# Performance work log

Measured on AMD Instinct MI355X. Metric: run time of the kernel, lower is better.

## Reference

```python
import jax, jax.numpy as jnp
import numpy as np

B, T, E = 64, 512, 768
H = 512            # hid_dim
NF = 256           # n_filters
FS = (3, 4, 5)     # filter_sizes


def gru_step(x, h, Wih, Whh, bih, bhh):
    # torch.nn.GRUCell math; gate order: reset, update, new
    gi = x @ Wih.T + bih
    gh = h @ Whh.T + bhh
    ir, iz, in_ = jnp.split(gi, 3, axis=-1)
    hr, hz, hn = jnp.split(gh, 3, axis=-1)
    r = jax.nn.sigmoid(ir + hr)
    z = jax.nn.sigmoid(iz + hz)
    n = jnp.tanh(in_ + r * hn)
    return (1.0 - z) * n + z * h


def setup_inputs() -> dict:
    key = jax.random.key(0)
    ks = jax.random.split(key, 32)
    s = 0.02
    inp = {
        "embedded": jax.random.normal(ks[0], (B, T, E), jnp.float32),
        "mask": jnp.ones((B, T), jnp.int32),
        # select-policy GRUCell
        "Wih_c": jax.random.normal(ks[1], (3 * H, E)) * s,
        "Whh_c": jax.random.normal(ks[2], (3 * H, H)) * s,
        "bih_c": jnp.zeros((3 * H,)),
        "bhh_c": jnp.zeros((3 * H,)),
        "Ws": jax.random.normal(ks[3], (2, H)) * s,
        "bs": jnp.zeros((2,)),
        # 2-layer GRU
        "Wih0": jax.random.normal(ks[4], (3 * H, E)) * s,
        "Whh0": jax.random.normal(ks[5], (3 * H, H)) * s,
        "bih0": jnp.zeros((3 * H,)),
        "bhh0": jnp.zeros((3 * H,)),
        "Wih1": jax.random.normal(ks[6], (3 * H, H)) * s,
        "Whh1": jax.random.normal(ks[7], (3 * H, H)) * s,
        "bih1": jnp.zeros((3 * H,)),
        "bhh1": jnp.zeros((3 * H,)),
        # convs (OIHW)
        "Wc3": jax.random.normal(ks[8], (NF, 1, 3, H)) * s,
        "bc3": jnp.zeros((NF,)),
        "Wc4": jax.random.normal(ks[9], (NF, 1, 4, H)) * s,
        "bc4": jnp.zeros((NF,)),
        "Wc5": jax.random.normal(ks[10], (NF, 1, 5, H)) * s,
        "bc5": jnp.zeros((NF,)),
        # output linear
        "Wo": jax.random.normal(ks[11], (1, len(FS) * NF)) * s,
        "bo": jnp.zeros((1,)),
    }
    return inp


def reference(embedded, mask, Wih_c, Whh_c, bih_c, bhh_c, Ws, bs,
              Wih0, Whh0, bih0, bhh0, Wih1, Whh1, bih1, bhh1,
              Wc3, bc3, Wc4, bc4, Wc5, bc5, Wo, bo):
    b, t, _ = embedded.shape
    emb = jax.lax.stop_gradient(embedded)  # policy uses detached embeddings
    lens = mask.sum(axis=1).astype(jnp.int32)  # [B]

    # --- select_policy (eval mode: argmax selection), batched scan over time ---
    def sel_step(h, x_t):
        h = gru_step(x_t, h, Wih_c, Whh_c, bih_c, bhh_c)
        logits = h @ Ws.T + bs  # [B, 2]
        return h, jnp.argmax(logits, axis=-1).astype(jnp.int32)

    h0 = jnp.zeros((b, Whh_c.shape[1]), emb.dtype)
    _, ks = jax.lax.scan(sel_step, h0, jnp.swapaxes(emb, 0, 1))  # [T, B]
    sel = ks.T  # [B, T]
    t_idx = jnp.arange(t)[None, :]
    sel = jnp.where(t_idx == 0, 1, sel)                  # first token always kept
    sel = jnp.where(t_idx == lens[:, None] - 1, 1, sel)  # last valid token kept
    sel = jnp.where(t_idx >= lens[:, None], 0, sel)      # padding never kept
    nsel = sel.sum(axis=1)  # [B] lengths of compacted sequences

    # compact selected tokens to the front (stable argsort trick)
    order = jnp.argsort(1 - sel, axis=1, stable=True)  # [B, T]
    new_emb = jnp.take_along_axis(emb, order[:, :, None], axis=1)
    valid = t_idx < nsel[:, None]  # [B, T]
    new_emb = new_emb * valid[:, :, None].astype(emb.dtype)

    # --- 2-layer GRU over packed (= masked, left-aligned) sequences ---
    def run_layer(x, Wih, Whh, bih, bhh):
        def step(h, inputs):
            x_t, m_t = inputs
            hn = gru_step(x_t, h, Wih, Whh, bih, bhh)
            h = jnp.where(m_t[:, None], hn, h)
            return h, jnp.where(m_t[:, None], hn, jnp.zeros_like(hn))
        hh = jnp.zeros((x.shape[0], Whh.shape[1]), x.dtype)
        _, ys = jax.lax.scan(step, hh, (jnp.swapaxes(x, 0, 1), valid.T))
        return jnp.swapaxes(ys, 0, 1)  # [B, T, H]

    out = run_layer(new_emb, Wih0, Whh0, bih0, bhh0)
    out = run_layer(out, Wih1, Whh1, bih1, bhh1)

    # --- Kim-CNN head ---
    xc = out[:, None, :, :]  # [B, 1, T, H]
    pooled = []
    for Wc, bc in ((Wc3, bc3), (Wc4, bc4), (Wc5, bc5)):
        c = jax.lax.conv_general_dilated(
            xc, Wc, (1, 1), 'VALID',
            dimension_numbers=('NCHW', 'OIHW', 'NCHW'))  # [B, NF, T-fs+1, 1]
        c = jax.nn.relu(c + bc[None, :, None, None])[..., 0]
        pooled.append(jnp.max(c, axis=2))  # [B, NF]
    cat = jnp.concatenate(pooled, axis=1)  # dropout is identity in eval
    return (cat @ Wo.T + bo)[:, 0]  # [B]
```

## Files before the change

### kernel.cpp

```cpp
#include <hip/hip_runtime.h>
#include <hip/hip_bf16.h>
#include <cstddef>

constexpr int B_ = 64, T_ = 512, E_ = 768, H_ = 512, G_ = 1536, NF_ = 256;

typedef float f32x4 __attribute__((ext_vector_type(4)));
typedef __bf16 bf16x8 __attribute__((ext_vector_type(8)));

constexpr size_t SZ_GIC   = (size_t)B_ * T_ * G_ * 4;
constexpr size_t OFF_GI   = 0;
constexpr size_t OFF_OUT  = (size_t)B_ * T_ * G_ * 2;
constexpr size_t OFF_WBF0 = 170u * 1024 * 1024;
constexpr size_t OFF_WBF1 = OFF_WBF0 + (size_t)G_ * H_ * 2;
constexpr size_t OFF_WIH0 = OFF_WBF1 + (size_t)G_ * H_ * 2;
constexpr size_t OFF_WIH1 = OFF_WIH0 + (size_t)G_ * E_ * 2;
constexpr size_t OFF_WC3  = OFF_WIH1 + (size_t)G_ * H_ * 2;
constexpr size_t OFF_WC4  = OFF_WC3 + (size_t)NF_ * 3 * H_ * 2;
constexpr size_t OFF_WC5  = OFF_WC4 + (size_t)NF_ * 4 * H_ * 2;
constexpr size_t OFF_MISC = SZ_GIC;
constexpr size_t OFF_H0   = OFF_MISC;
constexpr size_t OFF_H1   = OFF_H0 + (size_t)B_ * H_ * 4;
constexpr size_t OFF_SEL  = OFF_H1 + (size_t)B_ * H_ * 4;
constexpr size_t OFF_ORD  = OFF_SEL + (size_t)B_ * T_ * 4;
constexpr size_t OFF_NSEL = OFF_ORD + (size_t)B_ * T_ * 4;
constexpr size_t OFF_MAXN = OFF_NSEL + 256;
constexpr size_t OFF_FLG  = OFF_MAXN + 256;
constexpr size_t OFF_POOL = OFF_FLG + 512;
constexpr size_t OFF_RING0 = OFF_POOL + (size_t)B_ * 3 * NF_ * 4;
constexpr size_t OFF_RING1 = OFF_RING0 + 4ull * 64 * 512 * 2;
constexpr size_t WS_NEED  = OFF_RING1 + 4ull * 64 * 1536 * 2;

constexpr int WP_N0 = G_ * H_;
constexpr int WP_N1 = WP_N0 + G_ * H_;
constexpr int WP_N2 = WP_N1 + G_ * E_;
constexpr int WP_N3 = WP_N2 + G_ * H_;
constexpr int WP_N4 = WP_N3 + NF_ * 3 * H_;
constexpr int WP_N5 = WP_N4 + NF_ * 4 * H_;
constexpr int WP_N6 = WP_N5 + NF_ * 5 * H_;

#define CLOAD4(dst, ptr) \
    asm volatile("global_load_dwordx4 %0, %1, off sc0 sc1" : "=v"(dst) : "v"(ptr))
#define CLOAD2(dst, ptr) \
    asm volatile("global_load_dwordx2 %0, %1, off sc0 sc1" : "=v"(dst) : "v"(ptr))
#define CWAIT() do { \
    asm volatile("s_waitcnt vmcnt(0)" ::: "memory"); \
    __builtin_amdgcn_sched_barrier(0); } while (0)
#define CSTORE4(ptr, val) \
    asm volatile("global_store_dword %0, %1, off sc0 sc1" :: "v"(ptr), "v"(val) : "memory")
#define CSTORE8(ptr, val) \
    asm volatile("global_store_dwordx2 %0, %1, off sc0 sc1" :: "v"(ptr), "v"(val) : "memory")
#define CSTORE2(ptr, val) \
    asm volatile("global_store_short %0, %1, off sc0 sc1" :: "v"(ptr), "v"(val) : "memory")

__device__ __forceinline__ float sigm(float x) { return 1.f / (1.f + expf(-x)); }
__device__ __forceinline__ float b2f(unsigned short u) {
    return __uint_as_float(((unsigned int)u) << 16);
}
__device__ __forceinline__ unsigned short f2bu(float x) {
    __hip_bfloat16 h = __float2bfloat16(x);
    return *(unsigned short*)&h;
}

template<int NWG>
__device__ __forceinline__ void bar_wait(const int* flags, int t, int tid) {
    if (tid < 64) {
        int v;
        for (;;) {
            asm volatile("global_load_dword %0, %1, off sc0 sc1\n\t"
                         "s_waitcnt vmcnt(0)"
                         : "=v"(v) : "v"(flags + (tid & (NWG - 1))) : "memory");
            if (__all(v >= t)) break;
            __builtin_amdgcn_s_sleep(1);
        }
    }
    __syncthreads();
}

template<int N>
__device__ __forceinline__ void poll_ge(const int* flags, int thresh, int tid) {
    if (tid < 64) {
        const int idx = (tid < N) ? tid : 0;
        int v;
        for (;;) {
            asm volatile("global_load_dword %0, %1, off sc0 sc1\n\t"
                         "s_waitcnt vmcnt(0)"
                         : "=v"(v) : "v"(flags + idx) : "memory");
            if (__all(v >= thresh)) break;
            __builtin_amdgcn_s_sleep(1);
        }
    }
    __syncthreads();
}

__device__ __forceinline__ void bar_wait128(const int* flags, int t, int tid) {
    if (tid < 64) {
        int v1, v2;
        for (;;) {
            asm volatile("global_load_dword %0, %2, off sc0 sc1\n\t"
                         "global_load_dword %1, %3, off sc0 sc1\n\t"
                         "s_waitcnt vmcnt(0)"
                         : "=&v"(v1), "=&v"(v2)
                         : "v"(flags + tid), "v"(flags + tid + 64) : "memory");
            if (__all((v1 >= t) && (v2 >= t))) break;
            __builtin_amdgcn_s_sleep(1);
        }
    }
    __syncthreads();
}

__device__ __forceinline__ void bar_arrive(int* flags, int t, int tid, int idx) {
    asm volatile("s_waitcnt vmcnt(0)" ::: "memory");
    __syncthreads();
    if (tid == 0) { int pv = t + 1; CSTORE4(flags + idx, pv); }
}

__global__ __launch_bounds__(256) void gemm_f32(
    const float* __restrict__ A, const float* __restrict__ W,
    const float* __restrict__ bias, float* __restrict__ Cf,
    int N, int K, int ldA)
{
    __shared__ float As[16 * 68];
    __shared__ float Bs[16 * 68];
    const int tid = threadIdx.x;
    const int tx = tid & 15, ty = tid >> 4;
    const int id = blockIdx.x;
    const int sup = id / 384, rr = id % 384;
    const int bx = sup * 16 + (rr & 15);
    const int n0 = (rr >> 4) * 64;

    float acc[4][4] = {};
    const int rl = tid >> 2, kl = (tid & 3) * 4;
    const float* __restrict__ ap = A + ((size_t)bx * 64 + rl) * (size_t)ldA + kl;
    const float* __restrict__ wrow = W + (size_t)(n0 + rl) * (size_t)K + kl;

    for (int k0 = 0; k0 < K; k0 += 16) {
        float4 av = *(const float4*)(ap + k0);
        float4 wv = *(const float4*)(wrow + k0);
        __syncthreads();
        As[(kl+0)*68+rl] = av.x; As[(kl+1)*68+rl] = av.y;
        As[(kl+2)*68+rl] = av.z; As[(kl+3)*68+rl] = av.w;
        Bs[(kl+0)*68+rl] = wv.x; Bs[(kl+1)*68+rl] = wv.y;
        Bs[(kl+2)*68+rl] = wv.z; Bs[(kl+3)*68+rl] = wv.w;
        __syncthreads();
        #pragma unroll
        for (int kk = 0; kk < 16; ++kk) {
            const float4 a4 = *(const float4*)&As[kk*68 + ty*4];
            const float4 w4 = *(const float4*)&Bs[kk*68 + tx*4];
            acc[0][0]=fmaf(a4.x,w4.x,acc[0][0]); acc[0][1]=fmaf(a4.x,w4.y,acc[0][1]);
            acc[0][2]=fmaf(a4.x,w4.z,acc[0][2]); acc[0][3]=fmaf(a4.x,w4.w,acc[0][3]);
            acc[1][0]=fmaf(a4.y,w4.x,acc[1][0]); acc[1][1]=fmaf(a4.y,w4.y,acc[1][1]);
            acc[1][2]=fmaf(a4.y,w4.z,acc[1][2]); acc[1][3]=fmaf(a4.y,w4.w,acc[1][3]);
            acc[2][0]=fmaf(a4.z,w4.x,acc[2][0]); acc[2][1]=fmaf(a4.z,w4.y,acc[2][1]);
            acc[2][2]=fmaf(a4.z,w4.z,acc[2][2]); acc[2][3]=fmaf(a4.z,w4.w,acc[2][3]);
            acc[3][0]=fmaf(a4.w,w4.x,acc[3][0]); acc[3][1]=fmaf(a4.w,w4.y,acc[3][1]);
            acc[3][2]=fmaf(a4.w,w4.z,acc[3][2]); acc[3][3]=fmaf(a4.w,w4.w,acc[3][3]);
        }
    }
    #pragma unroll
    for (int i = 0; i < 4; ++i) {
        int m = bx * 64 + ty*4 + i;
        size_t co = (size_t)m * (size_t)N + n0 + tx*4;
        #pragma unroll
        for (int j = 0; j < 4; ++j)
            Cf[co + j] = acc[i][j] + bias[n0 + tx*4 + j];
    }
}

template<int AMODE, int OMODE>
__global__ __launch_bounds__(256) void gemm_mfma(
    const float* __restrict__ A, const unsigned short* __restrict__ Wb,
    const float* __restrict__ bias,
    unsigned short* __restrict__ Cb, unsigned int* __restrict__ pool,
    int N, int K, int ldA, int rowsPerB, int tilesPerB, int nb,
    const int* __restrict__ order, const int* __restrict__ nsel, int poolOff)
{
    __shared__ __align__(16) unsigned short As[64][40];
    __shared__ __align__(16) unsigned short Bs[64][40];
    __shared__ const float* rowp[64];

    const int tid = threadIdx.x;
    const int l = tid & 63;
    const int q = tid >> 6;
    const int per = 16 * nb;
    const int id = blockIdx.x;
    const int sup = id / per, rr2 = id % per;
    const int mblk = sup * 16 + (rr2 & 15);
    const int n0 = (rr2 >> 4) * 64;

    int tileb = 0, tilet0 = 0;
    if (AMODE != 0) { tileb = mblk / tilesPerB; tilet0 = (mblk % tilesPerB) * 64; }

    if (tid < 64) {
        const float* p = nullptr;
        if (AMODE == 0) {
            p = A + ((size_t)mblk * 64 + tid) * (size_t)ldA;
        } else if (AMODE == 1) {
            int t = tilet0 + tid;
            if (t < nsel[tileb]) {
                int src = order[tileb * T_ + t];
                p = A + ((size_t)tileb * T_ + src) * (size_t)ldA;
            }
        } else {
            int t = tilet0 + tid;
            if (t < rowsPerB) p = A + ((size_t)tileb * T_ + t) * (size_t)ldA;
        }
        rowp[tid] = p;
    }
    __syncthreads();

    f32x4 acc0 = {0.f,0.f,0.f,0.f}, acc1 = {0.f,0.f,0.f,0.f};
    f32x4 acc2 = {0.f,0.f,0.f,0.f}, acc3 = {0.f,0.f,0.f,0.f};

    const int r = tid & 63, seg = tid >> 6;
    const float* ap = rowp[r];
    if (ap) ap += seg * 8;
    const unsigned short* wrow = Wb + (size_t)(n0 + r) * (size_t)K + seg * 8;

    for (int k0 = 0; k0 < K; k0 += 32) {
        float4 fa = make_float4(0,0,0,0), fb = make_float4(0,0,0,0);
        if (ap) { fa = *(const float4*)(ap + k0); fb = *(const float4*)(ap + k0 + 4); }
        const uint4 wv = *(const uint4*)(wrow + k0);
        __syncthreads();
        uint4 pk;
        pk.x = (unsigned)f2bu(fa.x) | ((unsigned)f2bu(fa.y) << 16);
        pk.y = (unsigned)f2bu(fa.z) | ((unsigned)f2bu(fa.w) << 16);
        pk.z = (unsigned)f2bu(fb.x) | ((unsigned)f2bu(fb.y) << 16);
        pk.w = (unsigned)f2bu(fb.z) | ((unsigned)f2bu(fb.w) << 16);
        *(uint4*)&As[r][seg * 8] = pk;
        *(uint4*)&Bs[r][seg * 8] = wv;
        __syncthreads();
        const bf16x8 av = *(const bf16x8*)&As[q * 16 + (l & 15)][(l >> 4) * 8];
        const bf16x8 b0 = *(const bf16x8*)&Bs[ 0 + (l & 15)][(l >> 4) * 8];
        const bf16x8 b1 = *(const bf16x8*)&Bs[16 + (l & 15)][(l >> 4) * 8];
        const bf16x8 b2 = *(const bf16x8*)&Bs[32 + (l & 15)][(l >> 4) * 8];
        const bf16x8 b3 = *(const bf16x8*)&Bs[48 + (l & 15)][(l >> 4) * 8];
        acc0 = __builtin_amdgcn_mfma_f32_16x16x32_bf16(av, b0, acc0, 0, 0, 0);
        acc1 = __builtin_amdgcn_mfma_f32_16x16x32_bf16(av, b1, acc1, 0, 0, 0);
        acc2 = __builtin_amdgcn_mfma_f32_16x16x32_bf16(av, b2, acc2, 0, 0, 0);
        acc3 = __builtin_amdgcn_mfma_f32_16x16x32_bf16(av, b3, acc3, 0, 0, 0);
    }

    f32x4 accs[4] = {acc0, acc1, acc2, acc3};
    if (OMODE == 0) {
        const int mbase = (AMODE == 0) ? mblk * 64 : tileb * T_ + tilet0;
        #pragma unroll
        for (int s = 0; s < 4; ++s) {
            const int col = n0 + s * 16 + (l & 15);
            const float bv = bias[col];
            #pragma unroll
            for (int reg = 0; reg < 4; ++reg) {
                const int m = mbase + q * 16 + (l >> 4) * 4 + reg;
                Cb[(size_t)m * (size_t)N + col] = f2bu(accs[s][reg] + bv);
            }
        }
    } else {
        #pragma unroll
        for (int s = 0; s < 4; ++s) {
            const int col = n0 + s * 16 + (l & 15);
            const float bv = bias[col];
            float mx = 0.f;
            #pragma unroll
            for (int reg = 0; reg < 4; ++reg) {
                const int t = tilet0 + q * 16 + (l >> 4) * 4 + reg;
                const float val = fmaxf(accs[s][reg] + bv, 0.f);
                if (t < rowsPerB) mx = fmaxf(mx, val);
            }
            mx = fmaxf(mx, __shfl_xor(mx, 16));
            mx = fmaxf(mx, __shfl_xor(mx, 32));
            if (l < 16)
                atomicMax(&pool[(size_t)tileb * (3*NF_) + poolOff + n0 + s*16 + l],
                          __float_as_uint(mx));
        }
    }
}

__global__ void wprep_all(
    const float* __restrict__ w0, const float* __restrict__ w1,
    const float* __restrict__ w2, const float* __restrict__ w3,
    const float* __restrict__ w4, const float* __restrict__ w5,
    const float* __restrict__ w6, unsigned short* __restrict__ o)
{
    const int i = blockIdx.x * 256 + threadIdx.x;
    if (i >= WP_N6) return;
    float v;
    if      (i < WP_N0) v = w0[i];
    else if (i < WP_N1) v = w1[i - WP_N0];
    else if (i < WP_N2) v = w2[i - WP_N1];
    else if (i < WP_N3) v = w3[i - WP_N2];
    else if (i < WP_N4) v = w4[i - WP_N3];
    else if (i < WP_N5) v = w5[i - WP_N4];
    else                v = w6[i - WP_N5];
    o[i] = f2bu(v);
}

__device__ __forceinline__ void gates_abs(
    const float* __restrict__ hs, int b, int base,
    const float* __restrict__ wR, const float* __restrict__ wZ,
    const float* __restrict__ wN,
    float& aR, float& aZ, float& aN)
{
    #pragma unroll 4
    for (int kq = 0; kq < 32; ++kq) {
        const int k = base + kq * 4;
        const float hv0 = hs[(k+0)*64 + b];
        const float hv1 = hs[(k+1)*64 + b];
        const float hv2 = hs[(k+2)*64 + b];
        const float hv3 = hs[(k+3)*64 + b];
        const float4 wr = *(const float4*)(wR + k);
        const float4 wz = *(const float4*)(wZ + k);
        const float4 wn = *(const float4*)(wN + k);
        aR = fmaf(hv0, wr.x, aR); aR = fmaf(hv1, wr.y, aR);
        aR = fmaf(hv2, wr.z, aR); aR = fmaf(hv3, wr.w, aR);
        aZ = fmaf(hv0, wz.x, aZ); aZ = fmaf(hv1, wz.y, aZ);
        aZ = fmaf(hv2, wz.z, aZ); aZ = fmaf(hv3, wz.w, aZ);
        aN = fmaf(hv0, wn.x, aN); aN = fmaf(hv1, wn.y, aN);
        aN = fmaf(hv2, wn.z, aN); aN = fmaf(hv3, wn.w, aN);
    }
}

__device__ __forceinline__ void dot_abs(
    const float* __restrict__ hs, int b, int base,
    const float* __restrict__ dWl, float& dot)
{
    #pragma unroll 4
    for (int kq = 0; kq < 16; ++kq) {
        const int k = base + kq * 4;
        const float hv0 = hs[(k+0)*64 + b];
        const float hv1 = hs[(k+1)*64 + b];
        const float hv2 = hs[(k+2)*64 + b];
        const float hv3 = hs[(k+3)*64 + b];
        const float4 dv = *(const float4*)(dWl + k);
        dot = fmaf(hv0, dv.x, dot); dot = fmaf(hv1, dv.y, dot);
        dot = fmaf(hv2, dv.z, dot); dot = fmaf(hv3, dv.w, dot);
    }
}

__global__ __launch_bounds__(512) void rec_sel(
    const float* __restrict__ giF,
    const float* __restrict__ Whh, const float* __restrict__ bhh,
    const float* __restrict__ Ws, const float* __restrict__ bs,
    float* __restrict__ h0, float* __restrict__ h1,
    unsigned long long* __restrict__ selm, int* __restrict__ flags)
{
    __shared__ float Wl[12 * 512];
    __shared__ float dWl[512];
    __shared__ float hs[512 * 64];
    __shared__ float partR[4 * 64], partZ[4 * 64], partN[4 * 64];
    __shared__ float pdot[8 * 64];

    const int tid = threadIdx.x;
    const int b = tid & 63;
    const int w = __builtin_amdgcn_readfirstlane(tid >> 6);
    const int u = w >> 1, s = w & 1;
    const int bx = blockIdx.x;
    const int iu = bx * 4 + u;

    for (int idx = tid; idx < 12 * 512; idx += 512) {
        int rr = idx >> 9, k = idx & 511;
        int ul = rr / 3, gate = rr - ul * 3;
        Wl[idx] = Whh[((size_t)gate * 512 + bx * 4 + ul) * 512 + k];
    }
    dWl[tid] = Ws[512 + tid] - Ws[tid];
    __syncthreads();

    const float bR = bhh[iu], bZ = bhh[512 + iu], bN = bhh[1024 + iu];
    const float db = bs[1] - bs[0];
    const float* __restrict__ wR = Wl + (u*3 + 0) * 512;
    const float* __restrict__ wZ = Wl + (u*3 + 1) * 512;
    const float* __restrict__ wN = Wl + (u*3 + 2) * 512;

    float pgR = 0.f, pgZ = 0.f, pgN = 0.f;
    if (s == 0) {
        pgR = giF[(size_t)b * T_ * G_ + iu];
        pgZ = giF[(size_t)b * T_ * G_ + 512 + iu];
        pgN = giF[(size_t)b * T_ * G_ + 1024 + iu];
    }

    for (int t = 0; t <= T_; ++t) {
        const bool comp = (t < T_);
        const float* hcur = (t & 1) ? h1 : h0;
        float* hnxt = (t & 1) ? h0 : h1;

        if (t > 0) bar_wait128(flags, t, tid);

        const float* hc = hcur + (size_t)tid * 4;
        float* hd = hs + tid * 4;
        float4 a0,a1,a2,a3,a4,a5,a6,a7,a8,a9,aa,ab,ac,ad,ae,af;
        CLOAD4(a0, hc +  0*2048); CLOAD4(a1, hc +  1*2048);
        CLOAD4(a2, hc +  2*2048); CLOAD4(a3, hc +  3*2048);
        CLOAD4(a4, hc +  4*2048); CLOAD4(a5, hc +  5*2048);
        CLOAD4(a6, hc +  6*2048); CLOAD4(a7, hc +  7*2048);
        CLOAD4(a8, hc +  8*2048); CLOAD4(a9, hc +  9*2048);
        CLOAD4(aa, hc + 10*2048); CLOAD4(ab, hc + 11*2048);
        CLOAD4(ac, hc + 12*2048); CLOAD4(ad, hc + 13*2048);
        CLOAD4(ae, hc + 14*2048); CLOAD4(af, hc + 15*2048);
        CWAIT();
        *(float4*)(hd +  0*2048) = a0; *(float4*)(hd +  1*2048) = a1;
        *(float4*)(hd +  2*2048) = a2; *(float4*)(hd +  3*2048) = a3;
        *(float4*)(hd +  4*2048) = a4; *(float4*)(hd +  5*2048) = a5;
        *(float4*)(hd +  6*2048) = a6; *(float4*)(hd +  7*2048) = a7;
        *(float4*)(hd +  8*2048) = a8; *(float4*)(hd +  9*2048) = a9;
        *(float4*)(hd + 10*2048) = aa; *(float4*)(hd + 11*2048) = ab;
        *(float4*)(hd + 12*2048) = ac; *(float4*)(hd + 13*2048) = ad;
        *(float4*)(hd + 14*2048) = ae; *(float4*)(hd + 15*2048) = af;
        __syncthreads();

        float aR = (s == 0) ? bR : 0.f;
        float aZ = (s == 0) ? bZ : 0.f;
        float aN = (s == 0) ? bN : 0.f;
        float dot = 0.f, hp = 0.f;

        if (comp) {
            gates_abs(hs, b, s * 128,       wR, wZ, wN, aR, aZ, aN);
            gates_abs(hs, b, 256 + s * 128, wR, wZ, wN, aR, aZ, aN);
            if (s == 0) hp = hs[iu * 64 + b];
        }
        dot_abs(hs, b, (w < 4) ? w * 64 : 256 + (w - 4) * 64, dWl, dot);

        if (comp && s == 1) {
            partR[u*64 + b] = aR; partZ[u*64 + b] = aZ; partN[u*64 + b] = aN;
        }
        pdot[w*64 + b] = dot;
        __syncthreads();

        if (comp && s == 0) {
            aR += partR[u*64 + b]; aZ += partZ[u*64 + b]; aN += partN[u*64 + b];
            const float r = sigm(pgR + aR);
            const float z = sigm(pgZ + aZ);
            const float n = tanhf(pgN + r * aN);
            const float hn = (1.f - z) * n + z * hp;
            const float* hdst = hnxt + (size_t)iu * 64 + b;
            CSTORE4(hdst, hn);
        }

        if (t < T_) {
            bar_arrive(flags, t, tid, bx);
            if (s == 0 && t + 1 < T_) {
                const float* gp = giF + ((size_t)b * T_ + t + 1) * G_;
                pgR = gp[iu]; pgZ = gp[512 + iu]; pgN = gp[1024 + iu];
            }
        }
        if (w == 0 && t >= 1) {
            float p = pdot[0*64 + b];
            p += pdot[1*64 + b]; p += pdot[2*64 + b]; p += pdot[3*64 + b];
            p += pdot[4*64 + b]; p += pdot[5*64 + b]; p += pdot[6*64 + b];
            p += pdot[7*64 + b];
            unsigned long long m = __ballot((p + db) > 0.f);
            if (tid == 0 && bx == 0) selm[t - 1] = m;
        }
    }
}

template<int ROLE>
__device__ __forceinline__ void layer_body(
    int wg, int tid,
    const unsigned short* __restrict__ gi0,
    const unsigned short* __restrict__ ring1,
    unsigned short* __restrict__ ring0,
    const unsigned short* __restrict__ wbf, const float* __restrict__ bhh,
    const int* __restrict__ nselp, const int* __restrict__ maxnp,
    unsigned short* __restrict__ hA, unsigned short* __restrict__ hB,
    float* __restrict__ outp,
    int* __restrict__ flagsSelf, const int* __restrict__ flagsB,
    unsigned char* ldsW, unsigned char* ldsH, float* gbuf)
{
    const int l = tid & 63;
    const int q = tid >> 6;
    const int i0 = wg * 16;
    const int b = tid & 63;

    for (int idx = tid; idx < 48 * 64; idx += 256) {
        const int r = idx >> 6, seg = idx & 63;
        const int tier = r >> 4, ul = r & 15;
        const float4 v = *(const float4*)((const char*)wbf
            + ((size_t)(tier * 512 + i0 + ul) * 512) * 2 + seg * 16);
        *(float4*)(ldsW + r * 1040 + seg * 16) = v;
    }
    const float4 bRv = *(const float4*)(bhh + i0 + 4 * q);
    const float4 bZv = *(const float4*)(bhh + 512 + i0 + 4 * q);
    const float4 bNv = *(const float4*)(bhh + 1024 + i0 + 4 * q);
    const int ns = nselp[b];
    const int TOTAL = *maxnp;

    const unsigned short* gbase = gi0 + (size_t)b * T_ * (size_t)G_ + i0 + 4 * q;
    uint2 gR, gZ, gN;
    if (ROLE == 0) {
        gR = *(const uint2*)(gbase);
        gZ = *(const uint2*)(gbase + 512);
        gN = *(const uint2*)(gbase + 1024);
    }
    __syncthreads();

    for (int t = 0; t < TOTAL; ++t) {
        const unsigned short* hcur = (t & 1) ? hB : hA;
        unsigned short* hnxt = (t & 1) ? hA : hB;

        if (t > 0) bar_wait<32>(flagsSelf, t, tid);
        if (ROLE == 0) {
            if (t >= 4) poll_ge<24>(flagsB, t - 3, tid);
        } else {
            poll_ge<24>(flagsB, t + 1, tid);
            const unsigned short* gp = ring1 + ((size_t)(t & 3) * 64 + b) * G_ + i0 + 4 * q;
            CLOAD2(gR, gp); CLOAD2(gZ, gp + 512); CLOAD2(gN, gp + 1024);
        }

        {
            const char* src = (const char*)hcur + tid * 256;
            float4 s0, s1, s2, s3, s4, s5, s6, s7, s8, s9, sa, sb_, sc, sd, se, sf;
            CLOAD4(s0, src + 0 * 16);  CLOAD4(s1, src + 1 * 16);
            CLOAD4(s2, src + 2 * 16);  CLOAD4(s3, src + 3 * 16);
            CLOAD4(s4, src + 4 * 16);  CLOAD4(s5, src + 5 * 16);
            CLOAD4(s6, src + 6 * 16);  CLOAD4(s7, src + 7 * 16);
            CLOAD4(s8, src + 8 * 16);  CLOAD4(s9, src + 9 * 16);
            CLOAD4(sa, src + 10 * 16); CLOAD4(sb_, src + 11 * 16);
            CLOAD4(sc, src + 12 * 16); CLOAD4(sd, src + 13 * 16);
            CLOAD4(se, src + 14 * 16); CLOAD4(sf, src + 15 * 16);
            CWAIT();
            char* dst = (char*)ldsH + (tid >> 2) * 1040 + (tid & 3) * 256;
            *(float4*)(dst + 0 * 16) = s0;  *(float4*)(dst + 1 * 16) = s1;
            *(float4*)(dst + 2 * 16) = s2;  *(float4*)(dst + 3 * 16) = s3;
            *(float4*)(dst + 4 * 16) = s4;  *(float4*)(dst + 5 * 16) = s5;
            *(float4*)(dst + 6 * 16) = s6;  *(float4*)(dst + 7 * 16) = s7;
            *(float4*)(dst + 8 * 16) = s8;  *(float4*)(dst + 9 * 16) = s9;
            *(float4*)(dst + 10 * 16) = sa; *(float4*)(dst + 11 * 16) = sb_;
            *(float4*)(dst + 12 * 16) = sc; *(float4*)(dst + 13 * 16) = sd;
            *(float4*)(dst + 14 * 16) = se; *(float4*)(dst + 15 * 16) = sf;
        }
        __syncthreads();

        f32x4 ac0 = {0.f, 0.f, 0.f, 0.f};
        f32x4 ac1 = {0.f, 0.f, 0.f, 0.f};
        f32x4 ac2 = {0.f, 0.f, 0.f, 0.f};
        {
            const char* ab2 = (const char*)ldsH + (q * 16 + (l & 15)) * 1040 + (l >> 4) * 16;
            const char* bb = (const char*)ldsW + (l & 15) * 1040 + (l >> 4) * 16;
            #pragma unroll
            for (int ks = 0; ks < 16; ++ks) {
                const bf16x8 av = *(const bf16x8*)(ab2 + ks * 64);
                const bf16x8 w0 = *(const bf16x8*)(bb + ks * 64);
                const bf16x8 w1 = *(const bf16x8*)(bb + 16 * 1040 + ks * 64);
                const bf16x8 w2 = *(const bf16x8*)(bb + 32 * 1040 + ks * 64);
                ac0 = __builtin_amdgcn_mfma_f32_16x16x32_bf16(av, w0, ac0, 0, 0, 0);
                ac1 = __builtin_amdgcn_mfma_f32_16x16x32_bf16(av, w1, ac1, 0, 0, 0);
                ac2 = __builtin_amdgcn_mfma_f32_16x16x32_bf16(av, w2, ac2, 0, 0, 0);
            }
        }
        {
            const int gcol = q * 16 + 4 * (l >> 4);
            const int grow = l & 15;
            #pragma unroll
            for (int r = 0; r < 4; ++r) {
                gbuf[grow * 66 + gcol + r]        = ac0[r];
                gbuf[(16 + grow) * 66 + gcol + r] = ac1[r];
                gbuf[(32 + grow) * 66 + gcol + r] = ac2[r];
            }
        }
        __syncthreads();

        {
            const ushort4 hp4 = *(const ushort4*)((const char*)ldsH
                                 + b * 1040 + (i0 + 4 * q) * 2);
            const unsigned short hpb[4] = {hp4.x, hp4.y, hp4.z, hp4.w};
            const float irv[4] = {b2f(gR.x & 0xffff), b2f(gR.x >> 16),
                                  b2f(gR.y & 0xffff), b2f(gR.y >> 16)};
            const float izv[4] = {b2f(gZ.x & 0xffff), b2f(gZ.x >> 16),
                                  b2f(gZ.y & 0xffff), b2f(gZ.y >> 16)};
            const float inv[4] = {b2f(gN.x & 0xffff), b2f(gN.x >> 16),
                                  b2f(gN.y & 0xffff), b2f(gN.y >> 16)};
            float4 o;
            unsigned short ob[4];
            #pragma unroll
            for (int j = 0; j < 4; ++j) {
                const int u2 = 4 * q + j;
                const float hr = gbuf[u2 * 66 + b]        + bRv[j];
                const float hz = gbuf[(16 + u2) * 66 + b] + bZv[j];
                const float hn = gbuf[(32 + u2) * 66 + b] + bNv[j];
                const float rr = sigm(irv[j] + hr);
                const float zz = sigm(izv[j] + hz);
                const float nn = tanhf(inv[j] + rr * hn);
                const float hpf = b2f(hpb[j]);
                float hv = (1.f - zz) * nn + zz * hpf;
                if (t >= ns) hv = hpf;
                ((float*)&o)[j] = hv;
                ob[j] = f2bu(hv);
            }
            uint2 hpk;
            hpk.x = (unsigned)ob[0] | ((unsigned)ob[1] << 16);
            hpk.y = (unsigned)ob[2] | ((unsigned)ob[3] << 16);
            if (ROLE == 0) {
                const unsigned short* rdst = ring0 + ((size_t)(t & 3) * 64 + b) * 512 + i0 + 4 * q;
                CSTORE8(rdst, hpk);
            } else {
                if (t < ns)
                    *(float4*)(outp + ((size_t)b * T_ + t) * 512 + i0 + 4 * q) = o;
            }
            const unsigned short* hdst = hnxt + (size_t)b * 512 + i0 + 4 * q;
            CSTORE8(hdst, hpk);
        }

        bar_arrive(flagsSelf, t, tid, wg);
        if (ROLE == 0 && t + 1 < TOTAL) {
            const unsigned short* gp = gbase + (size_t)(t + 1) * G_;
            gR = *(const uint2*)gp;
            gZ = *(const uint2*)(gp + 512);
            gN = *(const uint2*)(gp + 1024);
        }
    }
}

__global__ __launch_bounds__(256) void rec_fused(
    const unsigned short* __restrict__ gi0,
    const unsigned short* __restrict__ wbf0,
    const unsigned short* __restrict__ wbf1,
    const unsigned short* __restrict__ wih1b,
    const float* __restrict__ bhh0, const float* __restrict__ bhh1,
    const float* __restrict__ bih1,
    const int* __restrict__ nselp, const int* __restrict__ maxnp,
    unsigned short* __restrict__ h0A, unsigned short* __restrict__ h1A,
    unsigned short* __restrict__ h0C, unsigned short* __restrict__ h1C,
    unsigned short* __restrict__ ring0, unsigned short* __restrict__ ring1,
    float* __restrict__ outp,
    int* __restrict__ flagsA, int* __restrict__ flagsB, int* __restrict__ flagsC)
{
    __shared__ __align__(16) unsigned char ldsX[64 * 1040];
    __shared__ __align__(16) unsigned char ldsY[64 * 1040];
    __shared__ float gbuf[48 * 66];

    const int tid = threadIdx.x;
    const int bx = blockIdx.x;

    if (bx < 32) {
        layer_body<0>(bx, tid, gi0, nullptr, ring0, wbf0, bhh0, nselp, maxnp,
                      h0A, h1A, nullptr, flagsA, flagsB, ldsX, ldsY, gbuf);
    } else if (bx < 56) {
        const int wg = bx - 32;
        const int l = tid & 63;
        const int q = tid >> 6;
        const int n0 = wg * 64;

        for (int idx = tid; idx < 64 * 64; idx += 256) {
            const int r = idx >> 6, seg = idx & 63;
            const float4 v = *(const float4*)((const char*)wih1b
                + ((size_t)(n0 + r) * 512) * 2 + seg * 16);
            *(float4*)(ldsX + r * 1040 + seg * 16) = v;
        }
        float bv[4];
        #pragma unroll
        for (int s = 0; s < 4; ++s) bv[s] = bih1[n0 + s * 16 + (l & 15)];
        const int TOTAL = *maxnp;
        __syncthreads();

        for (int t = 0; t < TOTAL; ++t) {
            poll_ge<32>(flagsA, t + 1, tid);
            if (t >= 4) poll_ge<32>(flagsC, t - 3, tid);

            {
                const char* src = (const char*)ring0 + (size_t)(t & 3) * 65536 + tid * 256;
                float4 s0, s1, s2, s3, s4, s5, s6, s7, s8, s9, sa, sb_, sc, sd, se, sf;
                CLOAD4(s0, src + 0 * 16);  CLOAD4(s1, src + 1 * 16);
                CLOAD4(s2, src + 2 * 16);  CLOAD4(s3, src + 3 * 16);
                CLOAD4(s4, src + 4 * 16);  CLOAD4(s5, src + 5 * 16);
                CLOAD4(s6, src + 6 * 16);  CLOAD4(s7, src + 7 * 16);
                CLOAD4(s8, src + 8 * 16);  CLOAD4(s9, src + 9 * 16);
                CLOAD4(sa, src + 10 * 16); CLOAD4(sb_, src + 11 * 16);
                CLOAD4(sc, src + 12 * 16); CLOAD4(sd, src + 13 * 16);
                CLOAD4(se, src + 14 * 16); CLOAD4(sf, src + 15 * 16);
                CWAIT();
                char* dst = (char*)ldsY + (tid >> 2) * 1040 + (tid & 3) * 256;
                *(float4*)(dst + 0 * 16) = s0;  *(float4*)(dst + 1 * 16) = s1;
                *(float4*)(dst + 2 * 16) = s2;  *(float4*)(dst + 3 * 16) = s3;
                *(float4*)(dst + 4 * 16) = s4;  *(float4*)(dst + 5 * 16) = s5;
                *(float4*)(dst + 6 * 16) = s6;  *(float4*)(dst + 7 * 16) = s7;
                *(float4*)(dst + 8 * 16) = s8;  *(float4*)(dst + 9 * 16) = s9;
                *(float4*)(dst + 10 * 16) = sa; *(float4*)(dst + 11 * 16) = sb_;
                *(float4*)(dst + 12 * 16) = sc; *(float4*)(dst + 13 * 16) = sd;
                *(float4*)(dst + 14 * 16) = se; *(float4*)(dst + 15 * 16) = sf;
            }
            __syncthreads();

            f32x4 acc0 = {0.f,0.f,0.f,0.f}, acc1 = {0.f,0.f,0.f,0.f};
            f32x4 acc2 = {0.f,0.f,0.f,0.f}, acc3 = {0.f,0.f,0.f,0.f};
            {
                const char* ab2 = (const char*)ldsY + (q * 16 + (l & 15)) * 1040 + (l >> 4) * 16;
                const char* bb = (const char*)ldsX + (l & 15) * 1040 + (l >> 4) * 16;
                #pragma unroll
                for (int ks = 0; ks < 16; ++ks) {
                    const bf16x8 av = *(const bf16x8*)(ab2 + ks * 64);
                    const bf16x8 b0 = *(const bf16x8*)(bb + ks * 64);
                    const bf16x8 b1 = *(const bf16x8*)(bb + 16 * 1040 + ks * 64);
                    const bf16x8 b2 = *(const bf16x8*)(bb + 32 * 1040 + ks * 64);
                    const bf16x8 b3 = *(const bf16x8*)(bb + 48 * 1040 + ks * 64);
                    acc0 = __builtin_amdgcn_mfma_f32_16x16x32_bf16(av, b0, acc0, 0, 0, 0);
                    acc1 = __builtin_amdgcn_mfma_f32_16x16x32_bf16(av, b1, acc1, 0, 0, 0);
                    acc2 = __builtin_amdgcn_mfma_f32_16x16x32_bf16(av, b2, acc2, 0, 0, 0);
                    acc3 = __builtin_amdgcn_mfma_f32_16x16x32_bf16(av, b3, acc3, 0, 0, 0);
                }
            }
            f32x4 accs[4] = {acc0, acc1, acc2, acc3};
            #pragma unroll
            for (int s = 0; s < 4; ++s) {
                const int col = n0 + s * 16 + (l & 15);
                #pragma unroll
                for (int reg = 0; reg < 4; ++reg) {
                    const int m = q * 16 + (l >> 4) * 4 + reg;
                    const unsigned val = f2bu(accs[s][reg] + bv[s]);
                    const unsigned short* dst = ring1 + ((size_t)(t & 3) * 64 + m) * G_ + col;
                    CSTORE2(dst, val);
                }
            }
            bar_arrive(flagsB, t, tid, wg);
        }
    } else {
        layer_body<1>(bx - 56, tid, nullptr, ring1, nullptr, wbf1, bhh1, nselp, maxnp,
                      h0C, h1C, outp, flagsC, flagsB, ldsX, ldsY, gbuf);
    }
}

__global__ void build_order_k(const int* __restrict__ mask,
                              const unsigned long long* __restrict__ selm,
                              int* __restrict__ order, int* __restrict__ nsel,
                              int* __restrict__ maxn)
{
    const int b = threadIdx.x;
    int lens = 0;
    for (int t = 0; t < T_; ++t) lens += (mask[b * T_ + t] != 0);
    int cnt = 0;
    for (int t = 0; t < T_; ++t) {
        int s = (int)((selm[t] >> b) & 1ull);
        if (t == 0) s = 1;
        if (t == lens - 1) s = 1;
        if (t >= lens) s = 0;
        if (s) order[b * T_ + (cnt++)] = t;
    }
    nsel[b] = cnt;
    int c2 = cnt;
    for (int t = 0; t < T_; ++t) {
        int s = (int)((selm[t] >> b) & 1ull);
        if (t == 0) s = 1;
        if (t == lens - 1) s = 1;
        if (t >= lens) s = 0;
        if (!s) order[b * T_ + (c2++)] = t;
    }
    __shared__ int red[64];
    red[b] = cnt;
    __syncthreads();
    if (b == 0) {
        int m = 0;
        for (int qq = 0; qq < 64; ++qq) m = max(m, red[qq]);
        *maxn = m;
    }
}

__global__ void final_k(const unsigned int* __restrict__ pool,
                        const float* __restrict__ Wo, const float* __restrict__ bo,
                        float* __restrict__ out)
{
    const int b = threadIdx.x;
    float s = bo[0];
    for (int f = 0; f < 3 * NF_; ++f)
        s = fmaf(__uint_as_float(pool[b * (3*NF_) + f]), Wo[f], s);
    out[b] = s;
}

extern "C" void kernel_launch(void* const* d_in, const int* in_sizes, int n_in,
                              void* d_out, int out_size, void* d_ws, size_t ws_size,
                              hipStream_t stream)
{
    (void)in_sizes; (void)n_in; (void)out_size;
    const float* emb   = (const float*)d_in[0];
    const int*   mask  = (const int*)d_in[1];
    const float* Wih_c = (const float*)d_in[2];
    const float* Whh_c = (const float*)d_in[3];
    const float* bih_c = (const float*)d_in[4];
    const float* bhh_c = (const float*)d_in[5];
    const float* Ws    = (const float*)d_in[6];
    const float* bs    = (const float*)d_in[7];
    const float* Wih0  = (const float*)d_in[8];
    const float* Whh0  = (const float*)d_in[9];
    const float* bih0  = (const float*)d_in[10];
    const float* bhh0  = (const float*)d_in[11];
    const float* Wih1  = (const float*)d_in[12];
    const float* Whh1  = (const float*)d_in[13];
    const float* bih1  = (const float*)d_in[14];
    const float* bhh1  = (const float*)d_in[15];
    const float* Wc3   = (const float*)d_in[16];
    const float* bc3   = (const float*)d_in[17];
    const float* Wc4   = (const float*)d_in[18];
    const float* bc4   = (const float*)d_in[19];
    const float* Wc5   = (const float*)d_in[20];
    const float* bc5   = (const float*)d_in[21];
    const float* Wo    = (const float*)d_in[22];
    const float* bo    = (const float*)d_in[23];

    if (ws_size < WS_NEED) return;
    char* ws = (char*)d_ws;
    float*          giC    = (float*)(ws + OFF_GI);
    unsigned short* giB    = (unsigned short*)(ws + OFF_GI);
    float*          outbuf = (float*)(ws + OFF_OUT);
    unsigned short* wpack  = (unsigned short*)(ws + OFF_WBF0);
    unsigned short* wbf0   = (unsigned short*)(ws + OFF_WBF0);
    unsigned short* wbf1   = (unsigned short*)(ws + OFF_WBF1);
    unsigned short* wih0b  = (unsigned short*)(ws + OFF_WIH0);
    unsigned short* wih1b  = (unsigned short*)(ws + OFF_WIH1);
    unsigned short* wc3b   = (unsigned short*)(ws + OFF_WC3);
    unsigned short* wc4b   = (unsigned short*)(ws + OFF_WC4);
    unsigned short* wc5b   = (unsigned short*)(ws + OFF_WC5);
    float*          h0f    = (float*)(ws + OFF_H0);
    float*          h1f    = (float*)(ws + OFF_H1);
    unsigned short* h0A    = (unsigned short*)(ws + OFF_H0);
    unsigned short* h1A    = (unsigned short*)(ws + OFF_H0 + 65536);
    unsigned short* h0C    = (unsigned short*)(ws + OFF_H0 + 131072);
    unsigned short* h1C    = (unsigned short*)(ws + OFF_H0 + 196608);
    unsigned long long* selm = (unsigned long long*)(ws + OFF_SEL);
    int*            order  = (int*)(ws + OFF_ORD);
    int*            nsel   = (int*)(ws + OFF_NSEL);
    int*            maxn   = (int*)(ws + OFF_MAXN);
    int*            flagsA = (int*)(ws + OFF_FLG);
    int*            flagsB = (int*)(ws + OFF_FLG + 128);
    int*            flagsC = (int*)(ws + OFF_FLG + 256);
    unsigned int*   pool   = (unsigned int*)(ws + OFF_POOL);
    unsigned short* ring0  = (unsigned short*)(ws + OFF_RING0);
    unsigned short* ring1  = (unsigned short*)(ws + OFF_RING1);

    gemm_f32<<<dim3(12288), 256, 0, stream>>>(emb, Wih_c, bih_c, giC, G_, E_, E_);
    hipMemsetAsync(flagsA, 0, 512, stream);
    hipMemsetAsync(h0f, 0, (size_t)B_ * H_ * 4, stream);
    rec_sel<<<128, 512, 0, stream>>>(giC, Whh_c, bhh_c, Ws, bs, h0f, h1f, selm, flagsA);
    build_order_k<<<1, 64, 0, stream>>>(mask, selm, order, nsel, maxn);
    wprep_all<<<(WP_N6 + 255) / 256, 256, 0, stream>>>(Whh0, Whh1, Wih0, Wih1,
                                                       Wc3, Wc4, Wc5, wpack);
    gemm_mfma<1,0><<<dim3(512 * 24), 256, 0, stream>>>(emb, wih0b, bih0, giB, nullptr,
                                                       G_, E_, E_, T_, 8, 24, order, nsel, 0);
    hipMemsetAsync(flagsA, 0, 512, stream);
    hipMemsetAsync(h0A, 0, 65536, stream);
    hipMemsetAsync(h0C, 0, 65536, stream);
    hipMemsetAsync(outbuf, 0, (size_t)B_ * T_ * H_ * 4, stream);
    rec_fused<<<88, 256, 0, stream>>>(giB, wbf0, wbf1, wih1b, bhh0, bhh1, bih1,
                                      nsel, maxn, h0A, h1A, h0C, h1C,
                                      ring0, ring1, outbuf, flagsA, flagsB, flagsC);
    hipMemsetAsync(pool, 0, (size_t)B_ * 3 * NF_ * 4, stream);
    gemm_mfma<2,1><<<dim3(512 * 4), 256, 0, stream>>>(outbuf, wc3b, bc3, nullptr, pool,
                                                      NF_, 3*H_, H_, 510, 8, 4, nullptr, nullptr, 0);
    gemm_mfma<2,1><<<dim3(512 * 4), 256, 0, stream>>>(outbuf, wc4b, bc4, nullptr, pool,
                                                      NF_, 4*H_, H_, 509, 8, 4, nullptr, nullptr, 256);
    gemm_mfma<2,1><<<dim3(512 * 4), 256, 0, stream>>>(outbuf, wc5b, bc5, nullptr, pool,
                                                      NF_, 5*H_, H_, 508, 8, 4, nullptr, nullptr, 512);
    final_k<<<1, 64, 0, stream>>>(pool, Wo, bo, (float*)d_out);
}
```

Baseline: 10.59 ms.

## Overlap select-policy input GEMM with recurrence via producer blocks and chunk counters

Removes the separate fp32 input-projection GEMM launch and folds it into the select-policy recurrent kernel. 128 extra blocks compute giC in time-chunk order and signal each finished chunk through atomic counters. The 128 recurrent blocks poll those counters before reading each new 64-step chunk, so the projection overlaps the serial scan. The cost is co-residency and spin-wait risk, plus a smaller per-block GEMM tile running on fewer blocks than the old 12288-block launch.

```diff
diff --git a/kernel.cpp b/kernel.cpp
--- a/kernel.cpp
+++ b/kernel.cpp
@@ -25,7 +25,8 @@
 constexpr size_t OFF_NSEL = OFF_ORD + (size_t)B_ * T_ * 4;
 constexpr size_t OFF_MAXN = OFF_NSEL + 256;
 constexpr size_t OFF_FLG  = OFF_MAXN + 256;
-constexpr size_t OFF_POOL = OFF_FLG + 512;
+constexpr size_t OFF_JOBS = OFF_FLG + 512;
+constexpr size_t OFF_POOL = OFF_FLG + 1024;
 constexpr size_t OFF_RING0 = OFF_POOL + (size_t)B_ * 3 * NF_ * 4;
 constexpr size_t OFF_RING1 = OFF_RING0 + 4ull * 64 * 512 * 2;
 constexpr size_t WS_NEED  = OFF_RING1 + 4ull * 64 * 1536 * 2;
@@ -51,6 +52,8 @@
     asm volatile("global_store_dwordx2 %0, %1, off sc0 sc1" :: "v"(ptr), "v"(val) : "memory")
 #define CSTORE2(ptr, val) \
     asm volatile("global_store_short %0, %1, off sc0 sc1" :: "v"(ptr), "v"(val) : "memory")
+#define CSTOREX4(ptr, val) \
+    asm volatile("global_store_dwordx4 %0, %1, off sc0 sc1" :: "v"(ptr), "v"(val) : "memory")
 
 __device__ __forceinline__ float sigm(float x) { return 1.f / (1.f + expf(-x)); }
 __device__ __forceinline__ float b2f(unsigned short u) {
@@ -92,6 +95,17 @@
     __syncthreads();
 }
 
+__device__ __forceinline__ void poll_cnt(const int* p, int thr) {
+    int v;
+    for (;;) {
+        asm volatile("global_load_dword %0, %1, off sc0 sc1\n\t"
+                     "s_waitcnt vmcnt(0)"
+                     : "=v"(v) : "v"(p) : "memory");
+        if (__all(v >= thr)) break;
+        __builtin_amdgcn_s_sleep(1);
+    }
+}
+
 __device__ __forceinline__ void bar_wait128(const int* flags, int t, int tid) {
     if (tid < 64) {
         int v1, v2;
@@ -112,58 +126,6 @@
     asm volatile("s_waitcnt vmcnt(0)" ::: "memory");
     __syncthreads();
     if (tid == 0) { int pv = t + 1; CSTORE4(flags + idx, pv); }
-}
-
-__global__ __launch_bounds__(256) void gemm_f32(
-    const float* __restrict__ A, const float* __restrict__ W,
-    const float* __restrict__ bias, float* __restrict__ Cf,
-    int N, int K, int ldA)
-{
-    __shared__ float As[16 * 68];
-    __shared__ float Bs[16 * 68];
-    const int tid = threadIdx.x;
-    const int tx = tid & 15, ty = tid >> 4;
-    const int id = blockIdx.x;
-    const int sup = id / 384, rr = id % 384;
-    const int bx = sup * 16 + (rr & 15);
-    const int n0 = (rr >> 4) * 64;
-
-    float acc[4][4] = {};
-    const int rl = tid >> 2, kl = (tid & 3) * 4;
-    const float* __restrict__ ap = A + ((size_t)bx * 64 + rl) * (size_t)ldA + kl;
-    const float* __restrict__ wrow = W + (size_t)(n0 + rl) * (size_t)K + kl;
-
-    for (int k0 = 0; k0 < K; k0 += 16) {
-        float4 av = *(const float4*)(ap + k0);
-        float4 wv = *(const float4*)(wrow + k0);
-        __syncthreads();
-        As[(kl+0)*68+rl] = av.x; As[(kl+1)*68+rl] = av.y;
-        As[(kl+2)*68+rl] = av.z; As[(kl+3)*68+rl] = av.w;
-        Bs[(kl+0)*68+rl] = wv.x; Bs[(kl+1)*68+rl] = wv.y;
-        Bs[(kl+2)*68+rl] = wv.z; Bs[(kl+3)*68+rl] = wv.w;
-        __syncthreads();
-        #pragma unroll
-        for (int kk = 0; kk < 16; ++kk) {
-            const float4 a4 = *(const float4*)&As[kk*68 + ty*4];
-            const float4 w4 = *(const float4*)&Bs[kk*68 + tx*4];
-            acc[0][0]=fmaf(a4.x,w4.x,acc[0][0]); acc[0][1]=fmaf(a4.x,w4.y,acc[0][1]);
-            acc[0][2]=fmaf(a4.x,w4.z,acc[0][2]); acc[0][3]=fmaf(a4.x,w4.w,acc[0][3]);
-            acc[1][0]=fmaf(a4.y,w4.x,acc[1][0]); acc[1][1]=fmaf(a4.y,w4.y,acc[1][1]);
-            acc[1][2]=fmaf(a4.y,w4.z,acc[1][2]); acc[1][3]=fmaf(a4.y,w4.w,acc[1][3]);
-            acc[2][0]=fmaf(a4.z,w4.x,acc[2][0]); acc[2][1]=fmaf(a4.z,w4.y,acc[2][1]);
-            acc[2][2]=fmaf(a4.z,w4.z,acc[2][2]); acc[2][3]=fmaf(a4.z,w4.w,acc[2][3]);
-            acc[3][0]=fmaf(a4.w,w4.x,acc[3][0]); acc[3][1]=fmaf(a4.w,w4.y,acc[3][1]);
-            acc[3][2]=fmaf(a4.w,w4.z,acc[3][2]); acc[3][3]=fmaf(a4.w,w4.w,acc[3][3]);
-        }
-    }
-    #pragma unroll
-    for (int i = 0; i < 4; ++i) {
-        int m = bx * 64 + ty*4 + i;
-        size_t co = (size_t)m * (size_t)N + n0 + tx*4;
-        #pragma unroll
-        for (int j = 0; j < 4; ++j)
-            Cf[co + j] = acc[i][j] + bias[n0 + tx*4 + j];
-    }
 }
 
 template<int AMODE, int OMODE>
@@ -335,24 +297,88 @@
     }
 }
 
-__global__ __launch_bounds__(512) void rec_sel(
-    const float* __restrict__ giF,
+__global__ __launch_bounds__(512) void sel_fused(
+    const float* __restrict__ emb, const float* __restrict__ Wih_c,
+    const float* __restrict__ bih_c, float* __restrict__ giC,
     const float* __restrict__ Whh, const float* __restrict__ bhh,
     const float* __restrict__ Ws, const float* __restrict__ bs,
     float* __restrict__ h0, float* __restrict__ h1,
-    unsigned long long* __restrict__ selm, int* __restrict__ flags)
-{
-    __shared__ float Wl[12 * 512];
-    __shared__ float dWl[512];
-    __shared__ float hs[512 * 64];
-    __shared__ float partR[4 * 64], partZ[4 * 64], partN[4 * 64];
-    __shared__ float pdot[8 * 64];
-
+    unsigned long long* __restrict__ selm, int* __restrict__ flags,
+    int* __restrict__ jobs)
+{
+    __shared__ __align__(16) char smem[162816];
     const int tid = threadIdx.x;
+    const int bx = blockIdx.x;
+
+    if (bx >= 128) {
+        const int p = bx - 128;
+        float* As = (float*)smem;
+        float* Bs = As + 16 * 68;
+        const int half = tid >> 8;
+        const int t2 = tid & 255;
+        const int srl = t2 >> 2, skl = (t2 & 3) * 4;
+        const int ty = tid >> 4;
+        const int tx = tid & 15;
+
+        for (int c = 0; c < 8; ++c) {
+            for (int j = p; j < 1536; j += 128) {
+                const int b = j / 24, n = j % 24;
+                const int mblk = b * 8 + c;
+                const int n0 = n * 64;
+                const float* src = (half == 0)
+                    ? emb + ((size_t)mblk * 64 + srl) * (size_t)E_ + skl
+                    : Wih_c + ((size_t)(n0 + srl)) * (size_t)E_ + skl;
+                float* dl = (half == 0) ? As : Bs;
+
+                float acc[2][4] = {};
+                for (int k0 = 0; k0 < E_; k0 += 16) {
+                    const float4 v = *(const float4*)(src + k0);
+                    __syncthreads();
+                    dl[(skl+0)*68 + srl] = v.x; dl[(skl+1)*68 + srl] = v.y;
+                    dl[(skl+2)*68 + srl] = v.z; dl[(skl+3)*68 + srl] = v.w;
+                    __syncthreads();
+                    #pragma unroll
+                    for (int kk = 0; kk < 16; ++kk) {
+                        const float a0 = As[kk*68 + ty*2 + 0];
+                        const float a1 = As[kk*68 + ty*2 + 1];
+                        const float4 w4 = *(const float4*)&Bs[kk*68 + tx*4];
+                        acc[0][0]=fmaf(a0,w4.x,acc[0][0]); acc[0][1]=fmaf(a0,w4.y,acc[0][1]);
+                        acc[0][2]=fmaf(a0,w4.z,acc[0][2]); acc[0][3]=fmaf(a0,w4.w,acc[0][3]);
+                        acc[1][0]=fmaf(a1,w4.x,acc[1][0]); acc[1][1]=fmaf(a1,w4.y,acc[1][1]);
+                        acc[1][2]=fmaf(a1,w4.z,acc[1][2]); acc[1][3]=fmaf(a1,w4.w,acc[1][3]);
+                    }
+                }
+                const float4 bv = *(const float4*)(bih_c + n0 + tx*4);
+                f32x4 o0, o1;
+                o0[0] = acc[0][0]+bv.x; o0[1] = acc[0][1]+bv.y;
+                o0[2] = acc[0][2]+bv.z; o0[3] = acc[0][3]+bv.w;
+                o1[0] = acc[1][0]+bv.x; o1[1] = acc[1][1]+bv.y;
+                o1[2] = acc[1][2]+bv.z; o1[3] = acc[1][3]+bv.w;
+                const float* d0 = giC + (size_t)(mblk * 64 + ty*2) * (size_t)G_ + n0 + tx*4;
+                CSTOREX4(d0, o0);
+                CSTOREX4(d0 + G_, o1);
+                asm volatile("s_waitcnt vmcnt(0)" ::: "memory");
+                __syncthreads();
+                if (tid == 0)
+                    __hip_atomic_fetch_add(jobs + c, 1, __ATOMIC_RELAXED,
+                                           __HIP_MEMORY_SCOPE_AGENT);
+                __syncthreads();
+            }
+        }
+        return;
+    }
+
+    float* Wl    = (float*)smem;
+    float* dWl   = Wl + 6144;
+    float* hs    = dWl + 512;
+    float* partR = hs + 32768;
+    float* partZ = partR + 256;
+    float* partN = partZ + 256;
+    float* pdot  = partN + 256;
+
     const int b = tid & 63;
     const int w = __builtin_amdgcn_readfirstlane(tid >> 6);
     const int u = w >> 1, s = w & 1;
-    const int bx = blockIdx.x;
     const int iu = bx * 4 + u;
 
     for (int idx = tid; idx < 12 * 512; idx += 512) {
@@ -370,10 +396,18 @@
     const float* __restrict__ wN = Wl + (u*3 + 2) * 512;
 
     float pgR = 0.f, pgZ = 0.f, pgN = 0.f;
+    int ready_chunk = 0;
     if (s == 0) {
-        pgR = giF[(size_t)b * T_ * G_ + iu];
-        pgZ = giF[(size_t)b * T_ * G_ + 512 + iu];
-        pgN = giF[(size_t)b * T_ * G_ + 1024 + iu];
+        poll_cnt(jobs + 0, 1536);
+        ready_chunk = 1;
+        const float* gp = giC + (size_t)b * T_ * G_;
+        asm volatile("global_load_dword %0, %3, off sc0 sc1\n\t"
+                     "global_load_dword %1, %4, off sc0 sc1\n\t"
+                     "global_load_dword %2, %5, off sc0 sc1\n\t"
+                     "s_waitcnt vmcnt(0)"
+                     : "=&v"(pgR), "=&v"(pgZ), "=&v"(pgN)
+                     : "v"(gp + iu), "v"(gp + 512 + iu), "v"(gp + 1024 + iu)
+                     : "memory");
     }
 
     for (int t = 0; t <= T_; ++t) {
@@ -436,16 +470,24 @@
         if (t < T_) {
             bar_arrive(flags, t, tid, bx);
             if (s == 0 && t + 1 < T_) {
-                const float* gp = giF + ((size_t)b * T_ + t + 1) * G_;
-                pgR = gp[iu]; pgZ = gp[512 + iu]; pgN = gp[1024 + iu];
+                const int nc = (t + 1) >> 6;
+                if (nc >= ready_chunk) { poll_cnt(jobs + nc, 1536); ready_chunk = nc + 1; }
+                const float* gp = giC + ((size_t)b * T_ + t + 1) * G_;
+                asm volatile("global_load_dword %0, %3, off sc0 sc1\n\t"
+                             "global_load_dword %1, %4, off sc0 sc1\n\t"
+                             "global_load_dword %2, %5, off sc0 sc1\n\t"
+                             "s_waitcnt vmcnt(0)"
+                             : "=&v"(pgR), "=&v"(pgZ), "=&v"(pgN)
+                             : "v"(gp + iu), "v"(gp + 512 + iu), "v"(gp + 1024 + iu)
+                             : "memory");
             }
         }
         if (w == 0 && t >= 1) {
-            float p = pdot[0*64 + b];
-            p += pdot[1*64 + b]; p += pdot[2*64 + b]; p += pdot[3*64 + b];
-            p += pdot[4*64 + b]; p += pdot[5*64 + b]; p += pdot[6*64 + b];
-            p += pdot[7*64 + b];
-            unsigned long long m = __ballot((p + db) > 0.f);
+            float p2 = pdot[0*64 + b];
+            p2 += pdot[1*64 + b]; p2 += pdot[2*64 + b]; p2 += pdot[3*64 + b];
+            p2 += pdot[4*64 + b]; p2 += pdot[5*64 + b]; p2 += pdot[6*64 + b];
+            p2 += pdot[7*64 + b];
+            unsigned long long m = __ballot((p2 + db) > 0.f);
             if (tid == 0 && bx == 0) selm[t - 1] = m;
         }
     }
@@ -818,14 +860,15 @@
     int*            flagsA = (int*)(ws + OFF_FLG);
     int*            flagsB = (int*)(ws + OFF_FLG + 128);
     int*            flagsC = (int*)(ws + OFF_FLG + 256);
+    int*            jobs   = (int*)(ws + OFF_JOBS);
     unsigned int*   pool   = (unsigned int*)(ws + OFF_POOL);
     unsigned short* ring0  = (unsigned short*)(ws + OFF_RING0);
     unsigned short* ring1  = (unsigned short*)(ws + OFF_RING1);
 
-    gemm_f32<<<dim3(12288), 256, 0, stream>>>(emb, Wih_c, bih_c, giC, G_, E_, E_);
-    hipMemsetAsync(flagsA, 0, 512, stream);
+    hipMemsetAsync(flagsA, 0, 1024, stream);
     hipMemsetAsync(h0f, 0, (size_t)B_ * H_ * 4, stream);
-    rec_sel<<<128, 512, 0, stream>>>(giC, Whh_c, bhh_c, Ws, bs, h0f, h1f, selm, flagsA);
+    sel_fused<<<256, 512, 0, stream>>>(emb, Wih_c, bih_c, giC, Whh_c, bhh_c,
+                                       Ws, bs, h0f, h1f, selm, flagsA, jobs);
     build_order_k<<<1, 64, 0, stream>>>(mask, selm, order, nsel, maxn);
     wprep_all<<<(WP_N6 + 255) / 256, 256, 0, stream>>>(Whh0, Whh1, Wih0, Wih1,
                                                        Wc3, Wc4, Wc5, wpack);
```

Result: faster. 9.703 ms, median of 2 (-8.4%).
